# Kernel optimization log

Measured on AMD Instinct MI355X. Metric: run time of the kernel, lower is better.

The kernel has to match this reference:

```python
import jax, jax.numpy as jnp
import numpy as np

NUM_LAYERS = 2
# Z eigenvalue of each basis state index (bit0 = qubit 0 = MSB, bit1 = qubit 1)
_Z0 = jnp.array([1.0, 1.0, -1.0, -1.0], dtype=jnp.float32)
_Z1 = jnp.array([1.0, -1.0, 1.0, -1.0], dtype=jnp.float32)
_CNOT_PERM = jnp.array([0, 1, 3, 2])  # CNOT(control=0, target=1) permutes |10>,|11>


def setup_inputs() -> dict:
    key = jax.random.key(0)
    k1, k2 = jax.random.split(key)
    x = jax.random.uniform(k1, (8192, 56, 56), dtype=jnp.float32)
    params = jax.random.uniform(k2, (2,), dtype=jnp.float32)
    return {"x": x, "params": params}


def reference(x, params):
    # x: (N, H, W). Each 2x2 patch contributes its top-row pair (x[r,c], x[r,c+1]).
    p0 = x[:, ::2, ::2]   # (N, H//2, W//2) -> angle for qubit 0
    p1 = x[:, ::2, 1::2]  # (N, H//2, W//2) -> angle for qubit 1
    # torch: patch.max() is the max over the whole (N, 2) slice at each (r, c)
    m = jnp.maximum(p0, p1).max(axis=0)  # (H//2, W//2)
    t0 = jnp.pi * p0 / (m + 1e-8)
    t1 = jnp.pi * p1 / (m + 1e-8)

    # RY(t)|0> = cos(t/2)|0> + sin(t/2)|1>; product state amplitudes, index = 2*b0 + b1
    c0, s0 = jnp.cos(t0 * 0.5), jnp.sin(t0 * 0.5)
    c1, s1 = jnp.cos(t1 * 0.5), jnp.sin(t1 * 0.5)
    a = jnp.stack([c0 * c1, c0 * s1, s0 * c1, s0 * s1], axis=-1).astype(jnp.complex64)

    # RZ(p) = diag(e^{-ip/2}, e^{+ip/2}) on each qubit -> diagonal phase per basis state
    phase = jnp.exp(-0.5j * (params[0] * _Z0 + params[1] * _Z1)).astype(jnp.complex64)
    for _ in range(NUM_LAYERS):
        a = a * phase          # RZ(params[0]) on q0, RZ(params[1]) on q1
        a = a[..., _CNOT_PERM]  # CNOT(0 -> 1)

    probs = jnp.real(a * jnp.conj(a))           # (N, H//2, W//2, 4)
    z0 = jnp.einsum('nhwk,k->nhw', probs, _Z0)  # <Z_0> (analytic expectation)
    N = x.shape[0]
    return z0.reshape(N, -1)  # (N, (H//2)*(W//2)), row-major matches r-then-c loop
```

## Files before the change

kernel.cpp:

```cpp
#include <hip/hip_runtime.h>


namespace {

constexpr int IMG  = 3136;
constexpr int HW   = 784;
constexpr int NIMG = 8192;
constexpr int NB1  = 512;
constexpr int IPB  = NIMG / NB1;
constexpr int IPB2 = 128;
constexpr int NSL  = NIMG / IPB2;

__global__ __launch_bounds__(256) void k_partial(const float* __restrict__ x,
                                                 float* __restrict__ M) {
    const int t = threadIdx.x;
    const int b = blockIdx.x;

    const int h0 = t / 14,  w0 = t - h0 * 14,  o0 = h0 * 112 + w0 * 4;
    const int u1 = t + 256;
    const int h1 = u1 / 14, w1 = u1 - h1 * 14, o1 = h1 * 112 + w1 * 4;
    const bool a1 = (u1 < 392);

    float2 lm0 = make_float2(0.f, 0.f);
    float2 lm1 = make_float2(0.f, 0.f);

    const float* base = x + (size_t)b * IPB * IMG;
#pragma unroll 4
    for (int n = 0; n < IPB; ++n) {
        const float* p = base + (size_t)n * IMG;
        float4 v = *(const float4*)(p + o0);
        lm0.x = fmaxf(lm0.x, fmaxf(v.x, v.y));
        lm0.y = fmaxf(lm0.y, fmaxf(v.z, v.w));
        if (a1) {
            float4 w = *(const float4*)(p + o1);
            lm1.x = fmaxf(lm1.x, fmaxf(w.x, w.y));
            lm1.y = fmaxf(lm1.y, fmaxf(w.z, w.w));
        }
    }

    *(float2*)(M + (size_t)b * HW + 2 * t) = lm0;
    if (a1) *(float2*)(M + (size_t)b * HW + 2 * u1) = lm1;
}

__global__ __launch_bounds__(256) void k_out(const float* __restrict__ x,
                                             const float* __restrict__ M,
                                             float* __restrict__ out) {
    __shared__ float part[8][28];

    const int bid = blockIdx.x;
    const int h   = bid % 28;
    const int n0  = (bid / 28) * IPB2;
    const int t   = threadIdx.x;
    const int c   = t % 28;
    const int g   = t / 28;
    const bool act = (t < 224);

    float p0[16];
    if (act) {
        const float* xp = x + (size_t)(n0 + g) * IMG + h * 112 + c * 2;
#pragma unroll
        for (int k = 0; k < 16; ++k)
            p0[k] = xp[(size_t)(8 * k) * IMG];

        const float* mp = M + (size_t)(g * 64) * HW + h * 28 + c;
        float cm = 0.0f;
#pragma unroll 8
        for (int r = 0; r < 64; ++r)
            cm = fmaxf(cm, mp[(size_t)r * HW]);
        part[g][c] = cm;
    }

    __syncthreads();

    if (act) {
        float m = part[0][c];
#pragma unroll
        for (int g2 = 1; g2 < 8; ++g2) m = fmaxf(m, part[g2][c]);
        const float r = 0.5f / (m + 1e-8f);

        float* op = out + (size_t)(n0 + g) * HW + h * 28 + c;
#pragma unroll
        for (int k = 0; k < 16; ++k)
            op[(size_t)(8 * k) * HW] = __builtin_amdgcn_cosf(p0[k] * r);
    }
}

}

extern "C" void kernel_launch(void* const* d_in, const int* in_sizes, int n_in,
                              void* d_out, int out_size, void* d_ws, size_t ws_size,
                              hipStream_t stream) {
    const float* x   = (const float*)d_in[0];
    float*       M   = (float*)d_ws;
    float*       out = (float*)d_out;

    hipLaunchKernelGGL(k_partial, dim3(NB1), dim3(256), 0, stream, x, M);
    hipLaunchKernelGGL(k_out, dim3(28 * NSL), dim3(256), 0, stream,
                       x, (const float*)M, out);
}
```

Measured before the change: 43.84 us.

## Fuse max-reduction and output into one persistent kernel with grid barriers

Merges the two kernels into a single 256-block kernel. Each block keeps its loaded x values in registers, writes partial maxima, syncs through a software grid barrier, reduces the maxima with atomicMax on float bits, syncs again, then computes the cosines without reading x a second time. This removes the second pass over x and one kernel launch, but adds a memset, two spin-wait barriers that assume all blocks are co-resident, and register pressure from 32-element arrays per thread.

```diff
diff --git a/kernel.cpp b/kernel.cpp
--- a/kernel.cpp
+++ b/kernel.cpp
@@ -6,13 +6,25 @@
 constexpr int IMG  = 3136;
 constexpr int HW   = 784;
 constexpr int NIMG = 8192;
-constexpr int NB1  = 512;
-constexpr int IPB  = NIMG / NB1;
-constexpr int IPB2 = 128;
-constexpr int NSL  = NIMG / IPB2;
+constexpr int NB   = 256;
+constexpr int IPB  = NIMG / NB;
 
-__global__ __launch_bounds__(256) void k_partial(const float* __restrict__ x,
-                                                 float* __restrict__ M) {
+__device__ __forceinline__ void grid_barrier(unsigned* cnt, unsigned target) {
+    __syncthreads();
+    if (threadIdx.x == 0) {
+        __threadfence();
+        __hip_atomic_fetch_add(cnt, 1u, __ATOMIC_ACQ_REL, __HIP_MEMORY_SCOPE_AGENT);
+        while (__hip_atomic_load(cnt, __ATOMIC_ACQUIRE, __HIP_MEMORY_SCOPE_AGENT) < target)
+            __builtin_amdgcn_s_sleep(2);
+    }
+    __syncthreads();
+}
+
+__global__ __launch_bounds__(256, 2)
+void k_all(const float* __restrict__ x, float* __restrict__ M,
+           unsigned* __restrict__ mu, unsigned* __restrict__ cnt,
+           float* __restrict__ out)
+{
     const int t = threadIdx.x;
     const int b = blockIdx.x;
 
@@ -21,67 +33,68 @@
     const int h1 = u1 / 14, w1 = u1 - h1 * 14, o1 = h1 * 112 + w1 * 4;
     const bool a1 = (u1 < 392);
 
-    float2 lm0 = make_float2(0.f, 0.f);
-    float2 lm1 = make_float2(0.f, 0.f);
+    float pa0[IPB], pa1[IPB], pb0[IPB], pb1[IPB];
+    float2 lm0 = make_float2(0.f, 0.f), lm1 = make_float2(0.f, 0.f);
 
     const float* base = x + (size_t)b * IPB * IMG;
-#pragma unroll 4
+#pragma unroll
     for (int n = 0; n < IPB; ++n) {
         const float* p = base + (size_t)n * IMG;
         float4 v = *(const float4*)(p + o0);
+        pa0[n] = v.x; pa1[n] = v.z;
         lm0.x = fmaxf(lm0.x, fmaxf(v.x, v.y));
         lm0.y = fmaxf(lm0.y, fmaxf(v.z, v.w));
         if (a1) {
             float4 w = *(const float4*)(p + o1);
+            pb0[n] = w.x; pb1[n] = w.z;
             lm1.x = fmaxf(lm1.x, fmaxf(w.x, w.y));
             lm1.y = fmaxf(lm1.y, fmaxf(w.z, w.w));
         }
     }
-
     *(float2*)(M + (size_t)b * HW + 2 * t) = lm0;
     if (a1) *(float2*)(M + (size_t)b * HW + 2 * u1) = lm1;
-}
 
-__global__ __launch_bounds__(256) void k_out(const float* __restrict__ x,
-                                             const float* __restrict__ M,
-                                             float* __restrict__ out) {
-    __shared__ float part[8][28];
+    grid_barrier(cnt + 0, NB);
 
-    const int bid = blockIdx.x;
-    const int h   = bid % 28;
-    const int n0  = (bid / 28) * IPB2;
-    const int t   = threadIdx.x;
-    const int c   = t % 28;
-    const int g   = t / 28;
-    const bool act = (t < 224);
-
-    float p0[16];
-    if (act) {
-        const float* xp = x + (size_t)(n0 + g) * IMG + h * 112 + c * 2;
+    {
+        const int u = b * 256 + t;
+        if (u < HW * 16) {
+            const int g = u / HW, col = u - g * HW;
+            const float* mp = M + (size_t)(g * 16) * HW + col;
+            float cm = 0.f;
 #pragma unroll
-        for (int k = 0; k < 16; ++k)
-            p0[k] = xp[(size_t)(8 * k) * IMG];
-
-        const float* mp = M + (size_t)(g * 64) * HW + h * 28 + c;
-        float cm = 0.0f;
-#pragma unroll 8
-        for (int r = 0; r < 64; ++r)
-            cm = fmaxf(cm, mp[(size_t)r * HW]);
-        part[g][c] = cm;
+            for (int r = 0; r < 16; ++r)
+                cm = fmaxf(cm, mp[(size_t)r * HW]);
+            atomicMax(mu + col, __float_as_uint(cm));
+        }
     }
 
-    __syncthreads();
+    grid_barrier(cnt + 1, NB);
 
-    if (act) {
-        float m = part[0][c];
+    const float* muf = (const float*)mu;
+    const float2 ma = *(const float2*)(muf + 2 * t);
+    const float ra0 = 0.5f / (ma.x + 1e-8f);
+    const float ra1 = 0.5f / (ma.y + 1e-8f);
+    float rb0 = 0.f, rb1 = 0.f;
+    if (a1) {
+        const float2 mb = *(const float2*)(muf + 2 * u1);
+        rb0 = 0.5f / (mb.x + 1e-8f);
+        rb1 = 0.5f / (mb.y + 1e-8f);
+    }
+
+    float* ob = out + (size_t)b * IPB * HW;
 #pragma unroll
-        for (int g2 = 1; g2 < 8; ++g2) m = fmaxf(m, part[g2][c]);
-        const float r = 0.5f / (m + 1e-8f);
-
-        float* op = out + (size_t)(n0 + g) * HW + h * 28 + c;
-#pragma unroll
-        for (int k = 0; k < 16; ++k)
-            op[(size_t)(8 * k) * HW] = __builtin_amdgcn_cosf(p0[k] * r);
+    for (int n = 0; n < IPB; ++n) {
+        float2 oa;
+        oa.x = __builtin_amdgcn_cosf(pa0[n] * ra0);
+        oa.y = __builtin_amdgcn_cosf(pa1[n] * ra1);
+        *(float2*)(ob + (size_t)n * HW + 2 * t) = oa;
+        if (a1) {
+            float2 ov;
+            ov.x = __builtin_amdgcn_cosf(pb0[n] * rb0);
+            ov.y = __builtin_amdgcn_cosf(pb1[n] * rb1);
+            *(float2*)(ob + (size_t)n * HW + 2 * u1) = ov;
+        }
     }
 }
 
@@ -90,11 +103,16 @@
 extern "C" void kernel_launch(void* const* d_in, const int* in_sizes, int n_in,
                               void* d_out, int out_size, void* d_ws, size_t ws_size,
                               hipStream_t stream) {
-    const float* x   = (const float*)d_in[0];
-    float*       M   = (float*)d_ws;
-    float*       out = (float*)d_out;
+    const float*  x   = (const float*)d_in[0];
+    float*        M   = (float*)d_ws;
+    unsigned*     mu  = (unsigned*)((char*)d_ws + (size_t)NB * HW * 4);
+    unsigned*     cnt = mu + HW;
+    float*        out = (float*)d_out;
 
-    hipLaunchKernelGGL(k_partial, dim3(NB1), dim3(256), 0, stream, x, M);
-    hipLaunchKernelGGL(k_out, dim3(28 * NSL), dim3(256), 0, stream,
-                       x, (const float*)M, out);
+    hipMemsetAsync(mu, 0, (HW + 2) * sizeof(unsigned), stream);
+
+    void* args[] = { (void*)&x, (void*)&M, (void*)&mu, (void*)&cnt, (void*)&out };
+    hipLaunchKernelGGL(k_all, dim3(NB), dim3(256), 0, stream,
+                       x, M, mu, cnt, out);
+    (void)args;
 }
```

New measurement: 68.31 us. +55.8%, slower.
